# Kernel tuning notes

Measured on AMD Instinct MI355X. Metric: run time of the kernel, lower is better.

## Reference

```python
import jax, jax.numpy as jnp
import numpy as np

N = 50000       # num entities
F_IN = 256      # input feature dim
H = 128         # hidden_dim (= per-head dim, concat=False)
HEADS = 4
L = 3           # num_layers
T = 3           # num edge types
E = 250000      # edges per type
NEG = 0.2       # leaky_relu slope (module + GATv2 default)


def setup_inputs() -> dict:
    key = jax.random.key(0)
    ks = jax.random.split(key, 10)
    s = 0.05
    return {
        "feat": jax.random.normal(ks[0], (N, F_IN), jnp.float32),
        "emb_table": jax.random.normal(ks[1], (N, H), jnp.float32),
        "proj_w": jax.random.normal(ks[2], (F_IN, H), jnp.float32) * s,
        "proj_b": jnp.zeros((H,), jnp.float32),
        "ln_g": jnp.ones((H,), jnp.float32),
        "ln_b": jnp.zeros((H,), jnp.float32),
        "skip_w": jnp.ones((L,), jnp.float32),
        "Wl": jax.random.normal(ks[3], (L, T, H, HEADS * H), jnp.float32) * s,
        "Wr": jax.random.normal(ks[4], (L, T, H, HEADS * H), jnp.float32) * s,
        "att": jax.random.normal(ks[5], (L, T, HEADS, H), jnp.float32) * s,
        "bias": jnp.zeros((L, T, H), jnp.float32),
        "edge_src": jax.random.randint(ks[6], (T, E), 0, N, jnp.int64),
        "edge_dst": jax.random.randint(ks[7], (T, E), 0, N, jnp.int64),
    }


def _layer_norm(x, g, b):
    mu = jnp.mean(x, axis=-1, keepdims=True)
    var = jnp.mean(jnp.square(x - mu), axis=-1, keepdims=True)
    return (x - mu) * jax.lax.rsqrt(var + 1e-5) * g + b


def _l2norm(x):
    n = jnp.sqrt(jnp.sum(jnp.square(x), axis=-1, keepdims=True))
    return x / jnp.maximum(n, 1e-12)


def _gatv2(x, wl, wr, a, b, src, dst):
    # x: [N,H]; wl,wr: [H, HEADS*H]; a: [HEADS,H]; src/dst: [E]
    xl = (x @ wl).reshape(N, HEADS, H)
    xr = (x @ wr).reshape(N, HEADS, H)
    m = xl[src] + xr[dst]                                   # [E,HEADS,H]
    e = jnp.sum(a * jax.nn.leaky_relu(m, NEG), axis=-1)     # [E,HEADS]
    # segment softmax over incoming edges per destination node
    emax = jax.lax.stop_gradient(jax.ops.segment_max(e, dst, num_segments=N))
    ex = jnp.exp(e - emax[dst])
    den = jax.ops.segment_sum(ex, dst, num_segments=N)      # [N,HEADS]
    alpha = ex / (den[dst] + 1e-16)                         # [E,HEADS]
    out = jax.ops.segment_sum(alpha[:, :, None] * xl[src], dst, num_segments=N)
    return jnp.mean(out, axis=1) + b                        # concat=False -> head mean


def reference(feat, emb_table, proj_w, proj_b, ln_g, ln_b, skip_w,
              Wl, Wr, att, bias, edge_src, edge_dst):
    h = jax.nn.leaky_relu(_layer_norm(feat @ proj_w + proj_b, ln_g, ln_b), NEG)
    ne = _l2norm(emb_table)                                 # normalize(embedding(arange(N)))
    x0 = 0.7 * h + 0.5 * ne
    x = x0
    for i in range(L):
        # HeteroConv(aggr='mean') over edge types, all on node type 'entity'
        per_type = [
            _gatv2(x, Wl[i, t], Wr[i, t], att[i, t], bias[i, t],
                   edge_src[t], edge_dst[t])
            for t in range(T)
        ]
        xu = jnp.mean(jnp.stack(per_type, axis=0), axis=0)
        alpha = jax.nn.sigmoid(skip_w[i])
        x = jax.nn.leaky_relu(xu, NEG) + alpha * x0          # dropout = identity (eval)
    return x
```

## Files before the change

kernel.cpp:

```cpp
#include <hip/hip_runtime.h>
#include <hip/hip_bf16.h>
#include <math.h>

#define N_NODES 50000
#define NOFF    50004
#define NBLK    49
#define F_IN    256
#define H       128
#define HEADS   4
#define HH      512
#define L_LAYERS 3
#define T_TYPES  3
#define E_EDGES  250000
#define NEG      0.2f

#define GEMM_RB  391
#define GEMM_GRID (GEMM_RB*8)

typedef __attribute__((ext_vector_type(8))) short short8_t;
typedef __attribute__((ext_vector_type(4))) float float4_t;
typedef __attribute__((ext_vector_type(2))) float float2_t;

__device__ __forceinline__ float leaky(float x) { return x > 0.f ? x : NEG * x; }

__device__ __forceinline__ unsigned int cvt_pk_bf16(float lo, float hi) {
    unsigned int d;
    asm("v_cvt_pk_bf16_f32 %0, %1, %2" : "=v"(d) : "v"(lo), "v"(hi));
    return d;
}

__device__ __forceinline__ unsigned short f2bf(float f) {
    return (unsigned short)cvt_pk_bf16(f, f);
}

__device__ __forceinline__ float bf2f(unsigned short u) {
    union { unsigned int i; float f; } v; v.i = ((unsigned)u) << 16; return v.f;
}

__device__ __forceinline__ float2_t pk_add(float2_t a, float2_t b) {
    float2_t d;
    asm("v_pk_add_f32 %0, %1, %2" : "=v"(d) : "v"(a), "v"(b));
    return d;
}
__device__ __forceinline__ float2_t pk_fma(float2_t a, float2_t b, float2_t c) {
    float2_t d;
    asm("v_pk_fma_f32 %0, %1, %2, %3" : "=v"(d) : "v"(a), "v"(b), "v"(c));
    return d;
}
__device__ __forceinline__ float2_t pk_abs(float2_t a) {
    union { float2_t f; unsigned int u[2]; } v; v.f = a;
    v.u[0] &= 0x7fffffffu;
    v.u[1] &= 0x7fffffffu;
    return v.f;
}

__device__ __forceinline__ float fast_exp2(float x) {
    return __builtin_amdgcn_exp2f(x);
}

template <int CTRL>
__device__ __forceinline__ float dpp_add(float x) {
    union { float f; int i; } a, b;
    a.f = x;
    b.i = __builtin_amdgcn_update_dpp(0, a.i, CTRL, 0xf, 0xf, true);
    return x + b.f;
}
__device__ __forceinline__ float row16_reduce(float p) {
    p = dpp_add<0xB1>(p);
    p = dpp_add<0x4E>(p);
    p = dpp_add<0x141>(p);
    p = dpp_add<0x140>(p);
    return p;
}

__device__ __forceinline__ void unpack_pk(uint4 q, float2_t* o) {
    union { unsigned int i; float f; } v;
    float2_t t;
    v.i = q.x << 16;         t.x = v.f;
    v.i = q.x & 0xffff0000u; t.y = v.f; o[0] = t;
    v.i = q.y << 16;         t.x = v.f;
    v.i = q.y & 0xffff0000u; t.y = v.f; o[1] = t;
    v.i = q.z << 16;         t.x = v.f;
    v.i = q.z & 0xffff0000u; t.y = v.f; o[2] = t;
    v.i = q.w << 16;         t.x = v.f;
    v.i = q.w & 0xffff0000u; t.y = v.f; o[3] = t;
}

__global__ void detect_kernel(const int* __restrict__ edst, int* __restrict__ flag) {
    __shared__ int s_any;
    if (threadIdx.x == 0) s_any = 0;
    __syncthreads();
    int a = 0;
    #pragma unroll
    for (int j = 0; j < 8; ++j) a |= edst[2 * (threadIdx.x * 8 + j) + 1];
    if (a) atomicOr(&s_any, 1);
    __syncthreads();
    if (threadIdx.x == 0) *flag = s_any ? 0 : 1;
}

__global__ void hist_kernel(const int* __restrict__ edst, int* __restrict__ counts,
                            const int* __restrict__ flag) {
    int idx = blockIdx.x * 256 + threadIdx.x;
    if (idx < T_TYPES * E_EDGES) {
        int sh = *flag;
        int t = idx / E_EDGES;
        int d = edst[(size_t)idx << sh];
        if ((unsigned)d < N_NODES)
            atomicAdd(&counts[t * N_NODES + d], 1);
    }
}

__global__ __launch_bounds__(256) void scan_a_kernel(const int* __restrict__ counts,
                                                     int* __restrict__ bsum) {
    const int b = blockIdx.x;
    const int t = b / NBLK, ch = b % NBLK;
    const int tid = threadIdx.x, lane = tid & 63;
    __shared__ int ws[4];
    const int* cnt = counts + t * N_NODES;
    int i0 = ch * 1024 + tid * 4;
    int s = 0;
    if (i0 + 3 < N_NODES) { int4 v = *(const int4*)(cnt + i0); s = v.x + v.y + v.z + v.w; }
    else { for (int j = 0; j < 4; ++j) { int i = i0 + j; if (i < N_NODES) s += cnt[i]; } }
    #pragma unroll
    for (int o = 32; o > 0; o >>= 1) s += __shfl_xor(s, o);
    if (lane == 0) ws[tid >> 6] = s;
    __syncthreads();
    if (tid == 0) bsum[b] = ws[0] + ws[1] + ws[2] + ws[3];
}

__global__ void scan_b_kernel(int* __restrict__ bsum, int* __restrict__ off) {
    int t = threadIdx.x;
    if (t < T_TYPES) {
        int run = 0;
        for (int c = 0; c < NBLK; ++c) { int v = bsum[t * NBLK + c]; bsum[t * NBLK + c] = run; run += v; }
        off[t * NOFF + N_NODES] = run;
    }
}

__global__ __launch_bounds__(256) void scan_c_kernel(const int* counts,
                                                     const int* __restrict__ bsum,
                                                     int* __restrict__ off,
                                                     int* cursor) {
    const int b = blockIdx.x;
    const int t = b / NBLK, ch = b % NBLK;
    const int tid = threadIdx.x, lane = tid & 63, w = tid >> 6;
    __shared__ int ws[4];
    const int* cnt = counts + t * N_NODES;
    int i0 = ch * 1024 + tid * 4;
    int v0 = 0, v1 = 0, v2 = 0, v3 = 0;
    if (i0 + 3 < N_NODES) { int4 v = *(const int4*)(cnt + i0); v0 = v.x; v1 = v.y; v2 = v.z; v3 = v.w; }
    else {
        if (i0     < N_NODES) v0 = cnt[i0];
        if (i0 + 1 < N_NODES) v1 = cnt[i0 + 1];
        if (i0 + 2 < N_NODES) v2 = cnt[i0 + 2];
        if (i0 + 3 < N_NODES) v3 = cnt[i0 + 3];
    }
    int s = v0 + v1 + v2 + v3;
    int x = s;
    #pragma unroll
    for (int o = 1; o < 64; o <<= 1) { int y = __shfl_up(x, o); if (lane >= o) x += y; }
    if (lane == 63) ws[w] = x;
    __syncthreads();
    int woff = 0;
    #pragma unroll
    for (int j = 0; j < 4; ++j) woff += (j < w) ? ws[j] : 0;
    int base = bsum[b] + woff + (x - s);
    int e0 = base, e1 = e0 + v0, e2 = e1 + v1, e3 = e2 + v2;
    if (i0 + 3 < N_NODES) {
        *(int4*)(off + t * NOFF + i0)       = make_int4(e0, e1, e2, e3);
        *(int4*)(cursor + t * N_NODES + i0) = make_int4(e0, e1, e2, e3);
    } else {
        if (i0     < N_NODES) { off[t * NOFF + i0]     = e0; cursor[t * N_NODES + i0]     = e0; }
        if (i0 + 1 < N_NODES) { off[t * NOFF + i0 + 1] = e1; cursor[t * N_NODES + i0 + 1] = e1; }
        if (i0 + 2 < N_NODES) { off[t * NOFF + i0 + 2] = e2; cursor[t * N_NODES + i0 + 2] = e2; }
        if (i0 + 3 < N_NODES) { off[t * NOFF + i0 + 3] = e3; cursor[t * N_NODES + i0 + 3] = e3; }
    }
}

__global__ void scatter_kernel(const int* __restrict__ esrc, const int* __restrict__ edst,
                               int* __restrict__ cursor, int* __restrict__ csrc,
                               const int* __restrict__ flag) {
    int idx = blockIdx.x * 256 + threadIdx.x;
    if (idx < T_TYPES * E_EDGES) {
        int sh = *flag;
        int t = idx / E_EDGES;
        int d = edst[(size_t)idx << sh];
        if ((unsigned)d >= N_NODES) return;
        int s = esrc[(size_t)idx << sh];
        if ((unsigned)s >= N_NODES) s = 0;
        int pos = atomicAdd(&cursor[t * N_NODES + d], 1);
        if ((unsigned)pos < E_EDGES)
            csrc[(size_t)t * E_EDGES + pos] = s;
    }
}

__global__ void wconv_kernel(const float* __restrict__ Wl, const float* __restrict__ Wr,
                             unsigned short* __restrict__ Wt) {
    int idx = blockIdx.x * 256 + threadIdx.x;
    if (idx >= L_LAYERS * T_TYPES * 1024 * H) return;
    int lt  = idx / (1024 * H);
    int rem = idx - lt * (1024 * H);
    int c   = rem / H;
    int k   = rem - c * H;
    float v = (c < HH) ? Wl[(size_t)lt * H * HH + (size_t)k * HH + c]
                       : Wr[(size_t)lt * H * HH + (size_t)k * HH + (c - HH)];
    Wt[idx] = f2bf(v);
}

__global__ void featconv_kernel(const float* __restrict__ feat,
                                unsigned short* __restrict__ fHi,
                                unsigned short* __restrict__ fLo) {
    size_t i = ((size_t)blockIdx.x * 256 + threadIdx.x) * 4;
    if (i >= (size_t)N_NODES * F_IN) return;
    float4 v = *(const float4*)(feat + i);
    ushort4 h, l;
    h.x = f2bf(v.x); l.x = f2bf(v.x - bf2f(h.x));
    h.y = f2bf(v.y); l.y = f2bf(v.y - bf2f(h.y));
    h.z = f2bf(v.z); l.z = f2bf(v.z - bf2f(h.z));
    h.w = f2bf(v.w); l.w = f2bf(v.w - bf2f(h.w));
    *(ushort4*)(fHi + i) = h;
    *(ushort4*)(fLo + i) = l;
}

__global__ void pconv_kernel(const float* __restrict__ pw,
                             unsigned short* __restrict__ pWtHi,
                             unsigned short* __restrict__ pWtLo) {
    int idx = blockIdx.x * 256 + threadIdx.x;
    if (idx >= H * F_IN) return;
    int c = idx / F_IN, k = idx - c * F_IN;
    float v = pw[(size_t)k * H + c];
    unsigned short hi = f2bf(v);
    pWtHi[idx] = hi;
    pWtLo[idx] = f2bf(v - bf2f(hi));
}

__device__ __forceinline__ void stage_tile(unsigned short* dst, const unsigned short* src,
                                           int rbase, int kbase, int tid, bool guardRows) {
    #pragma unroll
    for (int it = 0; it < 8; ++it) {
        int c = it * 256 + tid;
        int r = c >> 4, k8 = c & 15;
        int slot = (k8 ^ (r & 15)) * 8;
        uint4 v = make_uint4(0, 0, 0, 0);
        int row = rbase + r;
        if (!guardRows || row < N_NODES)
            v = *(const uint4*)(src + (size_t)row * 256 + kbase + k8 * 8);
        *(uint4*)(dst + r * 128 + slot) = v;
    }
}

__global__ __launch_bounds__(256) void init_gemm_kernel(
    const unsigned short* __restrict__ fHi, const unsigned short* __restrict__ fLo,
    const unsigned short* __restrict__ pWtHi, const unsigned short* __restrict__ pWtLo,
    float* __restrict__ proj)
{
    __shared__ unsigned short smem[32768];
    unsigned short* As = smem;
    unsigned short* Bs = smem + 16384;
    const int tid = threadIdx.x;
    const int nb = blockIdx.x * 128;

    const int wv = tid >> 6, lane = tid & 63;
    const int lm = lane & 15, kg = lane >> 4;
    const int wm = (wv & 1) * 64, wn = (wv >> 1) * 64;
    float4_t acc[4][4];
    #pragma unroll
    for (int i = 0; i < 4; ++i)
        #pragma unroll
        for (int j = 0; j < 4; ++j)
            acc[i][j] = (float4_t){0.f, 0.f, 0.f, 0.f};

    auto compute = [&]() {
        #pragma unroll
        for (int ks = 0; ks < 4; ++ks) {
            const int K8 = ks * 4 + kg;
            const int slot = (K8 ^ lm) * 8;
            short8_t a[4], b[4];
            #pragma unroll
            for (int i = 0; i < 4; ++i) {
                a[i] = *(const short8_t*)(As + (wm + i * 16 + lm) * 128 + slot);
                b[i] = *(const short8_t*)(Bs + (wn + i * 16 + lm) * 128 + slot);
            }
            #pragma unroll
            for (int i = 0; i < 4; ++i)
                #pragma unroll
                for (int j = 0; j < 4; ++j)
                    acc[i][j] = __builtin_amdgcn_mfma_f32_16x16x32_bf16(a[i], b[j], acc[i][j], 0, 0, 0);
        }
    };

    #pragma unroll
    for (int kh = 0; kh < 2; ++kh) {
        const int kbase = kh * 128;
        stage_tile(As, fHi, nb, kbase, tid, true);
        stage_tile(Bs, pWtHi, 0, kbase, tid, false);
        __syncthreads();
        compute();
        __syncthreads();
        stage_tile(Bs, pWtLo, 0, kbase, tid, false);
        __syncthreads();
        compute();
        __syncthreads();
        stage_tile(As, fLo, nb, kbase, tid, true);
        stage_tile(Bs, pWtHi, 0, kbase, tid, false);
        __syncthreads();
        compute();
        __syncthreads();
    }

    #pragma unroll
    for (int i = 0; i < 4; ++i) {
        #pragma unroll
        for (int r = 0; r < 4; ++r) {
            int node = nb + wm + i * 16 + kg * 4 + r;
            if (node < N_NODES) {
                #pragma unroll
                for (int j = 0; j < 4; ++j)
                    proj[(size_t)node * H + wn + j * 16 + lm] = acc[i][j][r];
            }
        }
    }
}

__global__ __launch_bounds__(128) void ln_combine_kernel(
    const float* __restrict__ proj, const float* __restrict__ emb,
    const float* __restrict__ pb, const float* __restrict__ g, const float* __restrict__ b,
    float* __restrict__ x0, unsigned short* __restrict__ xcurb)
{
    __shared__ float s0[2], s1[2];
    const int tid = threadIdx.x;
    const int nb = blockIdx.x * 8;
    const int c = tid;
    float acc[8];
    #pragma unroll
    for (int nn = 0; nn < 8; ++nn) {
        int node = nb + nn;
        acc[nn] = (node < N_NODES) ? proj[(size_t)node * H + c] : 0.f;
    }
    const float pbc = pb[c], gc = g[c], bc = b[c];
    for (int nn = 0; nn < 8; ++nn) {
        float v = acc[nn] + pbc;
        float sum = v, sq = v * v;
        for (int o = 32; o > 0; o >>= 1) { sum += __shfl_down(sum, o); sq += __shfl_down(sq, o); }
        if ((tid & 63) == 0) { s0[tid >> 6] = sum; s1[tid >> 6] = sq; }
        __syncthreads();
        float tot = s0[0] + s0[1], tq = s1[0] + s1[1];
        __syncthreads();
        float mu = tot * (1.f / H);
        float var = tq * (1.f / H) - mu * mu;
        acc[nn] = leaky((v - mu) * rsqrtf(var + 1e-5f) * gc + bc);
    }
    for (int nn = 0; nn < 8; ++nn) {
        int node = nb + nn;
        float ev = (node < N_NODES) ? emb[(size_t)node * H + c] : 0.f;
        float sq = ev * ev;
        for (int o = 32; o > 0; o >>= 1) sq += __shfl_down(sq, o);
        if ((tid & 63) == 0) s0[tid >> 6] = sq;
        __syncthreads();
        float nrm = sqrtf(s0[0] + s0[1]);
        __syncthreads();
        float nev = ev / fmaxf(nrm, 1e-12f);
        float xv = 0.7f * acc[nn] + 0.5f * nev;
        if (node < N_NODES) {
            x0[(size_t)node * H + c] = xv;
            xcurb[(size_t)node * H + c] = f2bf(xv);
        }
    }
}

__global__ __launch_bounds__(256) void gemm_mfma_kernel(
    const unsigned short* __restrict__ x,
    const unsigned short* __restrict__ Wt,
    unsigned short* __restrict__ XL, unsigned short* __restrict__ XR)
{
    __shared__ unsigned short smem[32768];
    unsigned short* As = smem;
    unsigned short* Bs = smem + 16384;
    const int tid = threadIdx.x;

    const int f    = blockIdx.x;
    const int g    = (f % 8) * GEMM_RB + (f / 8);
    const int rowb = g >> 3;
    const int colb = g & 7;
    const int nb = rowb * 128;
    const int cb = colb * 128;

    #pragma unroll
    for (int it = 0; it < 8; ++it) {
        int c = it * 256 + tid;
        int r = c >> 4;
        int k8 = c & 15;
        int slot = (k8 ^ (r & 15)) * 8;
        int node = nb + r;
        uint4 va = make_uint4(0, 0, 0, 0);
        if (node < N_NODES) va = *(const uint4*)(x + (size_t)node * H + k8 * 8);
        *(uint4*)(As + r * H + slot) = va;
        uint4 vb = *(const uint4*)(Wt + (size_t)(cb + r) * H + k8 * 8);
        *(uint4*)(Bs + r * H + slot) = vb;
    }
    __syncthreads();

    const int wv = tid >> 6, lane = tid & 63;
    const int lm = lane & 15, kg = lane >> 4;
    const int wm = (wv & 1) * 64, wn = (wv >> 1) * 64;
    float4_t acc[4][4];
    #pragma unroll
    for (int i = 0; i < 4; ++i)
        #pragma unroll
        for (int j = 0; j < 4; ++j)
            acc[i][j] = (float4_t){0.f, 0.f, 0.f, 0.f};

    #pragma unroll
    for (int ks = 0; ks < 4; ++ks) {
        const int K8 = ks * 4 + kg;
        const int slot = (K8 ^ lm) * 8;
        short8_t a[4], b[4];
        #pragma unroll
        for (int i = 0; i < 4; ++i) {
            a[i] = *(const short8_t*)(As + (wm + i * 16 + lm) * H + slot);
            b[i] = *(const short8_t*)(Bs + (wn + i * 16 + lm) * H + slot);
        }
        #pragma unroll
        for (int i = 0; i < 4; ++i)
            #pragma unroll
            for (int j = 0; j < 4; ++j)
                acc[i][j] = __builtin_amdgcn_mfma_f32_16x16x32_bf16(a[i], b[j], acc[i][j], 0, 0, 0);
    }
    __syncthreads();

    unsigned short* Cs = smem;
    #pragma unroll
    for (int i = 0; i < 4; ++i) {
        int row0 = wm + i * 16 + kg * 4;
        #pragma unroll
        for (int j = 0; j < 4; ++j) {
            int col = wn + j * 16 + lm;
            #pragma unroll
            for (int r = 0; r < 4; ++r)
                Cs[(row0 + r) * 136 + col] = f2bf(acc[i][j][r]);
        }
    }
    __syncthreads();

    unsigned short* O = (colb < 4) ? XL : XR;
    const int cbase = (colb < 4) ? cb : cb - HH;
    #pragma unroll
    for (int it = 0; it < 8; ++it) {
        int c = it * 256 + tid;
        int r = c >> 4, k8 = (c & 15) * 8;
        int node = nb + r;
        if (node < N_NODES)
            *(uint4*)(O + (size_t)node * HH + cbase + k8) = *(const uint4*)(Cs + r * 136 + k8);
    }
}

__global__ __launch_bounds__(64) void aggregate_kernel(
    const unsigned short* __restrict__ XL, const unsigned short* __restrict__ XR,
    const float* __restrict__ att_t, const float* __restrict__ bias_t,
    const int* __restrict__ off, const int* __restrict__ csrc,
    float* __restrict__ xacc, int first,
    int fin, const float* __restrict__ x0, const float* __restrict__ skipw,
    int li, int last, unsigned short* __restrict__ xcurb, float* __restrict__ out)
{
    const int lane = threadIdx.x;
    const int d = blockIdx.x;
    if (d >= N_NODES) return;
    const int jb = lane * 8;
    const float L2E = 1.4426950408889634f;

    float2_t rv[4], c1[4], c2[4], acc2[4];
    {
        uint4 q = *(const uint4*)(XR + (size_t)d * HH + jb);
        unpack_pk(q, rv);
        float4 u0 = *(const float4*)(att_t + jb);
        float4 u1 = *(const float4*)(att_t + jb + 4);
        float av[8] = {u0.x, u0.y, u0.z, u0.w, u1.x, u1.y, u1.z, u1.w};
        #pragma unroll
        for (int u = 0; u < 4; ++u) {
            c1[u] = (float2_t){0.6f * L2E * av[2 * u], 0.6f * L2E * av[2 * u + 1]};
            c2[u] = (float2_t){0.4f * L2E * av[2 * u], 0.4f * L2E * av[2 * u + 1]};
            acc2[u] = (float2_t){0.f, 0.f};
        }
    }
    float den = 0.f;

    const int e0 = off[d];
    const int cnt = off[d + 1] - e0;

    uint4 q0 = make_uint4(0, 0, 0, 0), q1 = q0;
    unsigned s2 = 0, s3 = 0;
    if (cnt > 0) q0 = *(const uint4*)(XL + (size_t)((unsigned)csrc[e0])     * HH + jb);
    if (cnt > 1) q1 = *(const uint4*)(XL + (size_t)((unsigned)csrc[e0 + 1]) * HH + jb);
    if (cnt > 2) s2 = (unsigned)csrc[e0 + 2];
    if (cnt > 3) s3 = (unsigned)csrc[e0 + 3];

    int e = 0;
    for (; e + 1 < cnt; e += 2) {
        float2_t lv0[4], lv1[4];
        unpack_pk(q0, lv0);
        unpack_pk(q1, lv1);
        if (e + 2 < cnt) q0 = *(const uint4*)(XL + (size_t)s2 * HH + jb);
        if (e + 3 < cnt) q1 = *(const uint4*)(XL + (size_t)s3 * HH + jb);
        if (e + 4 < cnt) s2 = (unsigned)csrc[e0 + e + 4];
        if (e + 5 < cnt) s3 = (unsigned)csrc[e0 + e + 5];

        float2_t p20 = (float2_t){0.f, 0.f};
        float2_t p21 = (float2_t){0.f, 0.f};
        #pragma unroll
        for (int u = 0; u < 4; ++u) {
            float2_t m0 = pk_add(lv0[u], rv[u]);
            float2_t m1 = pk_add(lv1[u], rv[u]);
            float2_t a0 = pk_abs(m0);
            float2_t a1 = pk_abs(m1);
            p20 = pk_fma(c1[u], m0, p20);
            p21 = pk_fma(c1[u], m1, p21);
            p20 = pk_fma(c2[u], a0, p20);
            p21 = pk_fma(c2[u], a1, p21);
        }
        float p0 = row16_reduce(p20.x + p20.y);
        float p1 = row16_reduce(p21.x + p21.y);
        float w0 = fast_exp2(p0);
        float w1 = fast_exp2(p1);
        den += w0 + w1;
        float2_t w20 = (float2_t){w0, w0};
        float2_t w21 = (float2_t){w1, w1};
        #pragma unroll
        for (int u = 0; u < 4; ++u) {
            acc2[u] = pk_fma(w20, lv0[u], acc2[u]);
            acc2[u] = pk_fma(w21, lv1[u], acc2[u]);
        }
    }
    if (e < cnt) {
        float2_t lv0[4];
        unpack_pk(q0, lv0);
        float2_t p20 = (float2_t){0.f, 0.f};
        #pragma unroll
        for (int u = 0; u < 4; ++u) {
            float2_t m0 = pk_add(lv0[u], rv[u]);
            float2_t a0 = pk_abs(m0);
            p20 = pk_fma(c1[u], m0, p20);
            p20 = pk_fma(c2[u], a0, p20);
        }
        float p0 = row16_reduce(p20.x + p20.y);
        float w0 = fast_exp2(p0);
        den += w0;
        float2_t w20 = (float2_t){w0, w0};
        #pragma unroll
        for (int u = 0; u < 4; ++u) acc2[u] = pk_fma(w20, lv0[u], acc2[u]);
    }

    float inv = 1.f / (den + 1e-16f);
    float o[8];
    #pragma unroll
    for (int u = 0; u < 4; ++u) { o[2 * u] = acc2[u].x; o[2 * u + 1] = acc2[u].y; }
    #pragma unroll
    for (int u = 0; u < 8; ++u) {
        float v = o[u] * inv;
        v += __shfl_xor(v, 16);
        v += __shfl_xor(v, 32);
        o[u] = v * 0.25f;
    }
    if (lane < 16) {
        float* dst = xacc + (size_t)d * H + jb;
        #pragma unroll
        for (int u = 0; u < 8; ++u) o[u] += bias_t[jb + u];
        if (!fin) {
            float4 o0 = make_float4(o[0], o[1], o[2], o[3]);
            float4 o1 = make_float4(o[4], o[5], o[6], o[7]);
            if (first) {
                *(float4*)dst = o0;
                *(float4*)(dst + 4) = o1;
            } else {
                float4 c0 = *(const float4*)dst, c1v = *(const float4*)(dst + 4);
                o0.x += c0.x; o0.y += c0.y; o0.z += c0.z; o0.w += c0.w;
                o1.x += c1v.x; o1.y += c1v.y; o1.z += c1v.z; o1.w += c1v.w;
                *(float4*)dst = o0;
                *(float4*)(dst + 4) = o1;
            }
        } else {
            float sw = 1.f / (1.f + __expf(-skipw[li]));
            float4 c0 = *(const float4*)dst, c1v = *(const float4*)(dst + 4);
            float a0 = c0.x + o[0], a1 = c0.y + o[1], a2 = c0.z + o[2], a3 = c0.w + o[3];
            float a4 = c1v.x + o[4], a5 = c1v.y + o[5], a6 = c1v.z + o[6], a7 = c1v.w + o[7];
            const float* z = x0 + (size_t)d * H + jb;
            float4 z0 = *(const float4*)z, z1 = *(const float4*)(z + 4);
            float r0 = leaky(a0 * (1.f / 3.f)) + sw * z0.x;
            float r1 = leaky(a1 * (1.f / 3.f)) + sw * z0.y;
            float r2 = leaky(a2 * (1.f / 3.f)) + sw * z0.z;
            float r3 = leaky(a3 * (1.f / 3.f)) + sw * z0.w;
            float r4 = leaky(a4 * (1.f / 3.f)) + sw * z1.x;
            float r5 = leaky(a5 * (1.f / 3.f)) + sw * z1.y;
            float r6 = leaky(a6 * (1.f / 3.f)) + sw * z1.z;
            float r7 = leaky(a7 * (1.f / 3.f)) + sw * z1.w;
            if (last) {
                float* op = out + (size_t)d * H + jb;
                *(float4*)op       = make_float4(r0, r1, r2, r3);
                *(float4*)(op + 4) = make_float4(r4, r5, r6, r7);
            } else {
                unsigned int w0 = cvt_pk_bf16(r0, r1);
                unsigned int w1 = cvt_pk_bf16(r2, r3);
                unsigned int w2 = cvt_pk_bf16(r4, r5);
                unsigned int w3 = cvt_pk_bf16(r6, r7);
                *(uint4*)(xcurb + (size_t)d * H + jb) = make_uint4(w0, w1, w2, w3);
            }
        }
    }
}

extern "C" void kernel_launch(void* const* d_in, const int* in_sizes, int n_in,
                              void* d_out, int out_size, void* d_ws, size_t ws_size,
                              hipStream_t stream)
{
    const float* feat   = (const float*)d_in[0];
    const float* emb    = (const float*)d_in[1];
    const float* proj_w = (const float*)d_in[2];
    const float* proj_b = (const float*)d_in[3];
    const float* ln_g   = (const float*)d_in[4];
    const float* ln_b   = (const float*)d_in[5];
    const float* skip_w = (const float*)d_in[6];
    const float* Wl     = (const float*)d_in[7];
    const float* Wr     = (const float*)d_in[8];
    const float* att    = (const float*)d_in[9];
    const float* bias   = (const float*)d_in[10];
    const int*   esrc   = (const int*)d_in[11];
    const int*   edst   = (const int*)d_in[12];
    float* out = (float*)d_out;

    char* p = (char*)d_ws;
    auto alloc = [&](size_t bytes) -> char* {
        char* r = p; p += (bytes + 255) & ~(size_t)255; return r;
    };
    float* x0             = (float*)alloc((size_t)N_NODES * H * 4);
    unsigned short* xcurb = (unsigned short*)alloc((size_t)N_NODES * H * 2);
    unsigned short* XL    = (unsigned short*)alloc((size_t)N_NODES * HH * 2);
    unsigned short* XR    = (unsigned short*)alloc((size_t)N_NODES * HH * 2);
    unsigned short* Wt    = (unsigned short*)alloc((size_t)L_LAYERS * T_TYPES * 1024 * H * 2);
    unsigned short* pWtHi = (unsigned short*)alloc((size_t)H * F_IN * 2);
    unsigned short* pWtLo = (unsigned short*)alloc((size_t)H * F_IN * 2);
    int* off    = (int*)alloc((size_t)T_TYPES * NOFF * 4);
    int* cursor = (int*)alloc((size_t)T_TYPES * N_NODES * 4);
    int* csrc   = (int*)alloc((size_t)T_TYPES * E_EDGES * 4);
    int* bsum   = (int*)alloc((size_t)T_TYPES * NBLK * 4);
    int* eflag  = (int*)alloc(256);
    float* xacc = out;

    float* proj          = (float*)XL;
    unsigned short* fHi  = XR;
    unsigned short* fLo  = XR + (size_t)N_NODES * F_IN;

    detect_kernel<<<1, 256, 0, stream>>>(edst, eflag);
    hipMemsetAsync(cursor, 0, (size_t)T_TYPES * N_NODES * 4, stream);
    hist_kernel<<<(T_TYPES * E_EDGES + 255) / 256, 256, 0, stream>>>(edst, cursor, eflag);
    scan_a_kernel<<<T_TYPES * NBLK, 256, 0, stream>>>(cursor, bsum);
    scan_b_kernel<<<1, 256, 0, stream>>>(bsum, off);
    scan_c_kernel<<<T_TYPES * NBLK, 256, 0, stream>>>(cursor, bsum, off, cursor);
    scatter_kernel<<<(T_TYPES * E_EDGES + 255) / 256, 256, 0, stream>>>(esrc, edst, cursor, csrc, eflag);

    wconv_kernel<<<(L_LAYERS * T_TYPES * 1024 * H + 255) / 256, 256, 0, stream>>>(Wl, Wr, Wt);
    featconv_kernel<<<((N_NODES * F_IN / 4) + 255) / 256, 256, 0, stream>>>(feat, fHi, fLo);
    pconv_kernel<<<(H * F_IN + 255) / 256, 256, 0, stream>>>(proj_w, pWtHi, pWtLo);
    init_gemm_kernel<<<(N_NODES + 127) / 128, 256, 0, stream>>>(fHi, fLo, pWtHi, pWtLo, proj);
    ln_combine_kernel<<<N_NODES / 8, 128, 0, stream>>>(proj, emb, proj_b, ln_g, ln_b, x0, xcurb);

    for (int i = 0; i < L_LAYERS; ++i) {
        for (int t = 0; t < T_TYPES; ++t) {
            const int lt = i * T_TYPES + t;
            const unsigned short* wt = Wt + (size_t)lt * 1024 * H;
            const float* at = att + (size_t)lt * HEADS * H;
            const float* bi = bias + (size_t)lt * H;
            gemm_mfma_kernel<<<GEMM_GRID, 256, 0, stream>>>(xcurb, wt, XL, XR);
            aggregate_kernel<<<N_NODES, 64, 0, stream>>>(
                XL, XR, at, bi, off + t * NOFF, csrc + (size_t)t * E_EDGES,
                xacc, (t == 0) ? 1 : 0,
                (t == T_TYPES - 1) ? 1 : 0, x0, skip_w, i,
                (i == L_LAYERS - 1) ? 1 : 0, xcurb, out);
        }
    }
}
```

Before: 1.095 ms.

## Merge preprocessing kernels into combined launches and fold scan_b into scan_c

Independent setup kernels are packed into three multi-role launches that dispatch on block index: feature, weight and projection-weight conversion plus edge-format detection; the init GEMM plus histogram; and layer-norm combine plus block-sum scan. The serial scan_b kernel is removed, so each scan_c block now sums its preceding block totals itself and the last block writes the end offset. The aim is fewer kernel launches and serial gaps in preprocessing, with unrelated work running concurrently. The cost is that mixed-role blocks share one LDS and register allocation, and the layer-norm part now runs 256-thread blocks covering 16 nodes.

```diff
diff --git a/kernel.cpp b/kernel.cpp
--- a/kernel.cpp
+++ b/kernel.cpp
@@ -17,6 +17,17 @@
 #define GEMM_RB  391
 #define GEMM_GRID (GEMM_RB*8)
 
+#define CA_FEAT  12500
+#define CA_WCONV 4608
+#define CA_PCONV 128
+#define CA_TOTAL (CA_FEAT + CA_WCONV + CA_PCONV + 1)
+#define CB_INIT  391
+#define CB_HIST  2930
+#define CB_TOTAL (CB_INIT + CB_HIST)
+#define CC_LN    3125
+#define CC_SCANA (T_TYPES*NBLK)
+#define CC_TOTAL (CC_LN + CC_SCANA)
+
 typedef __attribute__((ext_vector_type(8))) short short8_t;
 typedef __attribute__((ext_vector_type(4))) float float4_t;
 typedef __attribute__((ext_vector_type(2))) float float2_t;
@@ -86,65 +97,236 @@
     v.i = q.w & 0xffff0000u; t.y = v.f; o[3] = t;
 }
 
-__global__ void detect_kernel(const int* __restrict__ edst, int* __restrict__ flag) {
+__device__ __forceinline__ void stage_tile(unsigned short* dst, const unsigned short* src,
+                                           int rbase, int kbase, int tid, bool guardRows) {
+    #pragma unroll
+    for (int it = 0; it < 8; ++it) {
+        int c = it * 256 + tid;
+        int r = c >> 4, k8 = c & 15;
+        int slot = (k8 ^ (r & 15)) * 8;
+        uint4 v = make_uint4(0, 0, 0, 0);
+        int row = rbase + r;
+        if (!guardRows || row < N_NODES)
+            v = *(const uint4*)(src + (size_t)row * 256 + kbase + k8 * 8);
+        *(uint4*)(dst + r * 128 + slot) = v;
+    }
+}
+
+__global__ __launch_bounds__(256) void combo_a_kernel(
+    const float* __restrict__ feat, unsigned short* __restrict__ fHi, unsigned short* __restrict__ fLo,
+    const float* __restrict__ Wl, const float* __restrict__ Wr, unsigned short* __restrict__ Wt,
+    const float* __restrict__ pw, unsigned short* __restrict__ pWtHi, unsigned short* __restrict__ pWtLo,
+    const int* __restrict__ edst, int* __restrict__ flag)
+{
     __shared__ int s_any;
-    if (threadIdx.x == 0) s_any = 0;
-    __syncthreads();
-    int a = 0;
-    #pragma unroll
-    for (int j = 0; j < 8; ++j) a |= edst[2 * (threadIdx.x * 8 + j) + 1];
-    if (a) atomicOr(&s_any, 1);
-    __syncthreads();
-    if (threadIdx.x == 0) *flag = s_any ? 0 : 1;
-}
-
-__global__ void hist_kernel(const int* __restrict__ edst, int* __restrict__ counts,
-                            const int* __restrict__ flag) {
-    int idx = blockIdx.x * 256 + threadIdx.x;
-    if (idx < T_TYPES * E_EDGES) {
-        int sh = *flag;
-        int t = idx / E_EDGES;
-        int d = edst[(size_t)idx << sh];
-        if ((unsigned)d < N_NODES)
-            atomicAdd(&counts[t * N_NODES + d], 1);
-    }
-}
-
-__global__ __launch_bounds__(256) void scan_a_kernel(const int* __restrict__ counts,
-                                                     int* __restrict__ bsum) {
-    const int b = blockIdx.x;
-    const int t = b / NBLK, ch = b % NBLK;
-    const int tid = threadIdx.x, lane = tid & 63;
+    const int bid = blockIdx.x;
+    const int tid = threadIdx.x;
+    if (bid < CA_FEAT) {
+        size_t i = ((size_t)bid * 256 + tid) * 4;
+        float4 v = *(const float4*)(feat + i);
+        ushort4 h, l;
+        h.x = f2bf(v.x); l.x = f2bf(v.x - bf2f(h.x));
+        h.y = f2bf(v.y); l.y = f2bf(v.y - bf2f(h.y));
+        h.z = f2bf(v.z); l.z = f2bf(v.z - bf2f(h.z));
+        h.w = f2bf(v.w); l.w = f2bf(v.w - bf2f(h.w));
+        *(ushort4*)(fHi + i) = h;
+        *(ushort4*)(fLo + i) = l;
+    } else if (bid < CA_FEAT + CA_WCONV) {
+        int idx = (bid - CA_FEAT) * 256 + tid;
+        int lt  = idx / (1024 * H);
+        int rem = idx - lt * (1024 * H);
+        int c   = rem / H;
+        int k   = rem - c * H;
+        float v = (c < HH) ? Wl[(size_t)lt * H * HH + (size_t)k * HH + c]
+                           : Wr[(size_t)lt * H * HH + (size_t)k * HH + (c - HH)];
+        Wt[idx] = f2bf(v);
+    } else if (bid < CA_FEAT + CA_WCONV + CA_PCONV) {
+        int idx = (bid - CA_FEAT - CA_WCONV) * 256 + tid;
+        int c = idx / F_IN, k = idx - c * F_IN;
+        float v = pw[(size_t)k * H + c];
+        unsigned short hi = f2bf(v);
+        pWtHi[idx] = hi;
+        pWtLo[idx] = f2bf(v - bf2f(hi));
+    } else {
+        if (tid == 0) s_any = 0;
+        __syncthreads();
+        int a = 0;
+        #pragma unroll
+        for (int j = 0; j < 8; ++j) a |= edst[2 * (tid * 8 + j) + 1];
+        if (a) atomicOr(&s_any, 1);
+        __syncthreads();
+        if (tid == 0) *flag = s_any ? 0 : 1;
+    }
+}
+
+__device__ __forceinline__ void init_gemm_body(
+    unsigned short* smem,
+    const unsigned short* __restrict__ fHi, const unsigned short* __restrict__ fLo,
+    const unsigned short* __restrict__ pWtHi, const unsigned short* __restrict__ pWtLo,
+    float* __restrict__ proj, int bid, int tid)
+{
+    unsigned short* As = smem;
+    unsigned short* Bs = smem + 16384;
+    const int nb = bid * 128;
+
+    const int wv = tid >> 6, lane = tid & 63;
+    const int lm = lane & 15, kg = lane >> 4;
+    const int wm = (wv & 1) * 64, wn = (wv >> 1) * 64;
+    float4_t acc[4][4];
+    #pragma unroll
+    for (int i = 0; i < 4; ++i)
+        #pragma unroll
+        for (int j = 0; j < 4; ++j)
+            acc[i][j] = (float4_t){0.f, 0.f, 0.f, 0.f};
+
+    auto compute = [&]() {
+        #pragma unroll
+        for (int ks = 0; ks < 4; ++ks) {
+            const int K8 = ks * 4 + kg;
+            const int slot = (K8 ^ lm) * 8;
+            short8_t a[4], b[4];
+            #pragma unroll
+            for (int i = 0; i < 4; ++i) {
+                a[i] = *(const short8_t*)(As + (wm + i * 16 + lm) * 128 + slot);
+                b[i] = *(const short8_t*)(Bs + (wn + i * 16 + lm) * 128 + slot);
+            }
+            #pragma unroll
+            for (int i = 0; i < 4; ++i)
+                #pragma unroll
+                for (int j = 0; j < 4; ++j)
+                    acc[i][j] = __builtin_amdgcn_mfma_f32_16x16x32_bf16(a[i], b[j], acc[i][j], 0, 0, 0);
+        }
+    };
+
+    #pragma unroll
+    for (int kh = 0; kh < 2; ++kh) {
+        const int kbase = kh * 128;
+        stage_tile(As, fHi, nb, kbase, tid, true);
+        stage_tile(Bs, pWtHi, 0, kbase, tid, false);
+        __syncthreads();
+        compute();
+        __syncthreads();
+        stage_tile(Bs, pWtLo, 0, kbase, tid, false);
+        __syncthreads();
+        compute();
+        __syncthreads();
+        stage_tile(As, fLo, nb, kbase, tid, true);
+        stage_tile(Bs, pWtHi, 0, kbase, tid, false);
+        __syncthreads();
+        compute();
+        __syncthreads();
+    }
+
+    #pragma unroll
+    for (int i = 0; i < 4; ++i) {
+        #pragma unroll
+        for (int r = 0; r < 4; ++r) {
+            int node = nb + wm + i * 16 + kg * 4 + r;
+            if (node < N_NODES) {
+                #pragma unroll
+                for (int j = 0; j < 4; ++j)
+                    proj[(size_t)node * H + wn + j * 16 + lm] = acc[i][j][r];
+            }
+        }
+    }
+}
+
+__global__ __launch_bounds__(256) void combo_b_kernel(
+    const unsigned short* __restrict__ fHi, const unsigned short* __restrict__ fLo,
+    const unsigned short* __restrict__ pWtHi, const unsigned short* __restrict__ pWtLo,
+    float* __restrict__ proj,
+    const int* __restrict__ edst, int* __restrict__ counts, const int* __restrict__ flag)
+{
+    __shared__ unsigned short smem[32768];
+    const int bid = blockIdx.x;
+    const int tid = threadIdx.x;
+    if (bid < CB_INIT) {
+        init_gemm_body(smem, fHi, fLo, pWtHi, pWtLo, proj, bid, tid);
+    } else {
+        int idx = (bid - CB_INIT) * 256 + tid;
+        if (idx < T_TYPES * E_EDGES) {
+            int sh = *flag;
+            int t = idx / E_EDGES;
+            int d = edst[(size_t)idx << sh];
+            if ((unsigned)d < N_NODES)
+                atomicAdd(&counts[t * N_NODES + d], 1);
+        }
+    }
+}
+
+__global__ __launch_bounds__(256) void combo_c_kernel(
+    const float* __restrict__ proj, const float* __restrict__ emb,
+    const float* __restrict__ pb, const float* __restrict__ g, const float* __restrict__ b,
+    float* __restrict__ x0, unsigned short* __restrict__ xcurb,
+    const int* __restrict__ counts, int* __restrict__ bsum)
+{
+    __shared__ float s0[4], s1[4];
     __shared__ int ws[4];
-    const int* cnt = counts + t * N_NODES;
-    int i0 = ch * 1024 + tid * 4;
-    int s = 0;
-    if (i0 + 3 < N_NODES) { int4 v = *(const int4*)(cnt + i0); s = v.x + v.y + v.z + v.w; }
-    else { for (int j = 0; j < 4; ++j) { int i = i0 + j; if (i < N_NODES) s += cnt[i]; } }
-    #pragma unroll
-    for (int o = 32; o > 0; o >>= 1) s += __shfl_xor(s, o);
-    if (lane == 0) ws[tid >> 6] = s;
-    __syncthreads();
-    if (tid == 0) bsum[b] = ws[0] + ws[1] + ws[2] + ws[3];
-}
-
-__global__ void scan_b_kernel(int* __restrict__ bsum, int* __restrict__ off) {
-    int t = threadIdx.x;
-    if (t < T_TYPES) {
-        int run = 0;
-        for (int c = 0; c < NBLK; ++c) { int v = bsum[t * NBLK + c]; bsum[t * NBLK + c] = run; run += v; }
-        off[t * NOFF + N_NODES] = run;
-    }
-}
-
-__global__ __launch_bounds__(256) void scan_c_kernel(const int* counts,
-                                                     const int* __restrict__ bsum,
-                                                     int* __restrict__ off,
-                                                     int* cursor) {
+    const int bid = blockIdx.x;
+    const int tid = threadIdx.x;
+    if (bid < CC_LN) {
+        const int h = tid >> 7;
+        const int c = tid & 127;
+        const int wv = tid >> 6;
+        const int nb = bid * 16 + h * 8;
+        float acc[8];
+        #pragma unroll
+        for (int nn = 0; nn < 8; ++nn)
+            acc[nn] = proj[(size_t)(nb + nn) * H + c];
+        const float pbc = pb[c], gc = g[c], bc = b[c];
+        for (int nn = 0; nn < 8; ++nn) {
+            float v = acc[nn] + pbc;
+            float sum = v, sq = v * v;
+            for (int o = 32; o > 0; o >>= 1) { sum += __shfl_down(sum, o); sq += __shfl_down(sq, o); }
+            if ((tid & 63) == 0) { s0[wv] = sum; s1[wv] = sq; }
+            __syncthreads();
+            float tot = s0[2 * h] + s0[2 * h + 1], tq = s1[2 * h] + s1[2 * h + 1];
+            __syncthreads();
+            float mu = tot * (1.f / H);
+            float var = tq * (1.f / H) - mu * mu;
+            acc[nn] = leaky((v - mu) * rsqrtf(var + 1e-5f) * gc + bc);
+        }
+        for (int nn = 0; nn < 8; ++nn) {
+            int node = nb + nn;
+            float ev = emb[(size_t)node * H + c];
+            float sq = ev * ev;
+            for (int o = 32; o > 0; o >>= 1) sq += __shfl_down(sq, o);
+            if ((tid & 63) == 0) s0[wv] = sq;
+            __syncthreads();
+            float nrm = sqrtf(s0[2 * h] + s0[2 * h + 1]);
+            __syncthreads();
+            float nev = ev / fmaxf(nrm, 1e-12f);
+            float xv = 0.7f * acc[nn] + 0.5f * nev;
+            x0[(size_t)node * H + c] = xv;
+            xcurb[(size_t)node * H + c] = f2bf(xv);
+        }
+    } else {
+        const int sb = bid - CC_LN;
+        const int t = sb / NBLK, ch = sb % NBLK;
+        const int lane = tid & 63;
+        const int* cnt = counts + t * N_NODES;
+        int i0 = ch * 1024 + tid * 4;
+        int s = 0;
+        if (i0 + 3 < N_NODES) { int4 v = *(const int4*)(cnt + i0); s = v.x + v.y + v.z + v.w; }
+        else { for (int j = 0; j < 4; ++j) { int i = i0 + j; if (i < N_NODES) s += cnt[i]; } }
+        #pragma unroll
+        for (int o = 32; o > 0; o >>= 1) s += __shfl_xor(s, o);
+        if (lane == 0) ws[tid >> 6] = s;
+        __syncthreads();
+        if (tid == 0) bsum[sb] = ws[0] + ws[1] + ws[2] + ws[3];
+    }
+}
+
+__global__ __launch_bounds__(256) void scan_c2_kernel(const int* counts,
+                                                      const int* __restrict__ bsum,
+                                                      int* __restrict__ off,
+                                                      int* cursor) {
     const int b = blockIdx.x;
     const int t = b / NBLK, ch = b % NBLK;
     const int tid = threadIdx.x, lane = tid & 63, w = tid >> 6;
     __shared__ int ws[4];
+    int run = 0;
+    for (int c = 0; c < ch; ++c) run += bsum[t * NBLK + c];
     const int* cnt = counts + t * N_NODES;
     int i0 = ch * 1024 + tid * 4;
     int v0 = 0, v1 = 0, v2 = 0, v3 = 0;
@@ -164,7 +346,7 @@
     int woff = 0;
     #pragma unroll
     for (int j = 0; j < 4; ++j) woff += (j < w) ? ws[j] : 0;
-    int base = bsum[b] + woff + (x - s);
+    int base = run + woff + (x - s);
     int e0 = base, e1 = e0 + v0, e2 = e1 + v1, e3 = e2 + v2;
     if (i0 + 3 < N_NODES) {
         *(int4*)(off + t * NOFF + i0)       = make_int4(e0, e1, e2, e3);
@@ -175,6 +357,8 @@
         if (i0 + 2 < N_NODES) { off[t * NOFF + i0 + 2] = e2; cursor[t * N_NODES + i0 + 2] = e2; }
         if (i0 + 3 < N_NODES) { off[t * NOFF + i0 + 3] = e3; cursor[t * N_NODES + i0 + 3] = e3; }
     }
+    if (ch == NBLK - 1 && tid == 255)
+        off[t * NOFF + N_NODES] = run + woff + x;
 }
 
 __global__ void scatter_kernel(const int* __restrict__ esrc, const int* __restrict__ edst,
@@ -191,180 +375,6 @@
         int pos = atomicAdd(&cursor[t * N_NODES + d], 1);
         if ((unsigned)pos < E_EDGES)
             csrc[(size_t)t * E_EDGES + pos] = s;
-    }
-}
-
-__global__ void wconv_kernel(const float* __restrict__ Wl, const float* __restrict__ Wr,
-                             unsigned short* __restrict__ Wt) {
-    int idx = blockIdx.x * 256 + threadIdx.x;
-    if (idx >= L_LAYERS * T_TYPES * 1024 * H) return;
-    int lt  = idx / (1024 * H);
-    int rem = idx - lt * (1024 * H);
-    int c   = rem / H;
-    int k   = rem - c * H;
-    float v = (c < HH) ? Wl[(size_t)lt * H * HH + (size_t)k * HH + c]
-                       : Wr[(size_t)lt * H * HH + (size_t)k * HH + (c - HH)];
-    Wt[idx] = f2bf(v);
-}
-
-__global__ void featconv_kernel(const float* __restrict__ feat,
-                                unsigned short* __restrict__ fHi,
-                                unsigned short* __restrict__ fLo) {
-    size_t i = ((size_t)blockIdx.x * 256 + threadIdx.x) * 4;
-    if (i >= (size_t)N_NODES * F_IN) return;
-    float4 v = *(const float4*)(feat + i);
-    ushort4 h, l;
-    h.x = f2bf(v.x); l.x = f2bf(v.x - bf2f(h.x));
-    h.y = f2bf(v.y); l.y = f2bf(v.y - bf2f(h.y));
-    h.z = f2bf(v.z); l.z = f2bf(v.z - bf2f(h.z));
-    h.w = f2bf(v.w); l.w = f2bf(v.w - bf2f(h.w));
-    *(ushort4*)(fHi + i) = h;
-    *(ushort4*)(fLo + i) = l;
-}
-
-__global__ void pconv_kernel(const float* __restrict__ pw,
-                             unsigned short* __restrict__ pWtHi,
-                             unsigned short* __restrict__ pWtLo) {
-    int idx = blockIdx.x * 256 + threadIdx.x;
-    if (idx >= H * F_IN) return;
-    int c = idx / F_IN, k = idx - c * F_IN;
-    float v = pw[(size_t)k * H + c];
-    unsigned short hi = f2bf(v);
-    pWtHi[idx] = hi;
-    pWtLo[idx] = f2bf(v - bf2f(hi));
-}
-
-__device__ __forceinline__ void stage_tile(unsigned short* dst, const unsigned short* src,
-                                           int rbase, int kbase, int tid, bool guardRows) {
-    #pragma unroll
-    for (int it = 0; it < 8; ++it) {
-        int c = it * 256 + tid;
-        int r = c >> 4, k8 = c & 15;
-        int slot = (k8 ^ (r & 15)) * 8;
-        uint4 v = make_uint4(0, 0, 0, 0);
-        int row = rbase + r;
-        if (!guardRows || row < N_NODES)
-            v = *(const uint4*)(src + (size_t)row * 256 + kbase + k8 * 8);
-        *(uint4*)(dst + r * 128 + slot) = v;
-    }
-}
-
-__global__ __launch_bounds__(256) void init_gemm_kernel(
-    const unsigned short* __restrict__ fHi, const unsigned short* __restrict__ fLo,
-    const unsigned short* __restrict__ pWtHi, const unsigned short* __restrict__ pWtLo,
-    float* __restrict__ proj)
-{
-    __shared__ unsigned short smem[32768];
-    unsigned short* As = smem;
-    unsigned short* Bs = smem + 16384;
-    const int tid = threadIdx.x;
-    const int nb = blockIdx.x * 128;
-
-    const int wv = tid >> 6, lane = tid & 63;
-    const int lm = lane & 15, kg = lane >> 4;
-    const int wm = (wv & 1) * 64, wn = (wv >> 1) * 64;
-    float4_t acc[4][4];
-    #pragma unroll
-    for (int i = 0; i < 4; ++i)
-        #pragma unroll
-        for (int j = 0; j < 4; ++j)
-            acc[i][j] = (float4_t){0.f, 0.f, 0.f, 0.f};
-
-    auto compute = [&]() {
-        #pragma unroll
-        for (int ks = 0; ks < 4; ++ks) {
-            const int K8 = ks * 4 + kg;
-            const int slot = (K8 ^ lm) * 8;
-            short8_t a[4], b[4];
-            #pragma unroll
-            for (int i = 0; i < 4; ++i) {
-                a[i] = *(const short8_t*)(As + (wm + i * 16 + lm) * 128 + slot);
-                b[i] = *(const short8_t*)(Bs + (wn + i * 16 + lm) * 128 + slot);
-            }
-            #pragma unroll
-            for (int i = 0; i < 4; ++i)
-                #pragma unroll
-                for (int j = 0; j < 4; ++j)
-                    acc[i][j] = __builtin_amdgcn_mfma_f32_16x16x32_bf16(a[i], b[j], acc[i][j], 0, 0, 0);
-        }
-    };
-
-    #pragma unroll
-    for (int kh = 0; kh < 2; ++kh) {
-        const int kbase = kh * 128;
-        stage_tile(As, fHi, nb, kbase, tid, true);
-        stage_tile(Bs, pWtHi, 0, kbase, tid, false);
-        __syncthreads();
-        compute();
-        __syncthreads();
-        stage_tile(Bs, pWtLo, 0, kbase, tid, false);
-        __syncthreads();
-        compute();
-        __syncthreads();
-        stage_tile(As, fLo, nb, kbase, tid, true);
-        stage_tile(Bs, pWtHi, 0, kbase, tid, false);
-        __syncthreads();
-        compute();
-        __syncthreads();
-    }
-
-    #pragma unroll
-    for (int i = 0; i < 4; ++i) {
-        #pragma unroll
-        for (int r = 0; r < 4; ++r) {
-            int node = nb + wm + i * 16 + kg * 4 + r;
-            if (node < N_NODES) {
-                #pragma unroll
-                for (int j = 0; j < 4; ++j)
-                    proj[(size_t)node * H + wn + j * 16 + lm] = acc[i][j][r];
-            }
-        }
-    }
-}
-
-__global__ __launch_bounds__(128) void ln_combine_kernel(
-    const float* __restrict__ proj, const float* __restrict__ emb,
-    const float* __restrict__ pb, const float* __restrict__ g, const float* __restrict__ b,
-    float* __restrict__ x0, unsigned short* __restrict__ xcurb)
-{
-    __shared__ float s0[2], s1[2];
-    const int tid = threadIdx.x;
-    const int nb = blockIdx.x * 8;
-    const int c = tid;
-    float acc[8];
-    #pragma unroll
-    for (int nn = 0; nn < 8; ++nn) {
-        int node = nb + nn;
-        acc[nn] = (node < N_NODES) ? proj[(size_t)node * H + c] : 0.f;
-    }
-    const float pbc = pb[c], gc = g[c], bc = b[c];
-    for (int nn = 0; nn < 8; ++nn) {
-        float v = acc[nn] + pbc;
-        float sum = v, sq = v * v;
-        for (int o = 32; o > 0; o >>= 1) { sum += __shfl_down(sum, o); sq += __shfl_down(sq, o); }
-        if ((tid & 63) == 0) { s0[tid >> 6] = sum; s1[tid >> 6] = sq; }
-        __syncthreads();
-        float tot = s0[0] + s0[1], tq = s1[0] + s1[1];
-        __syncthreads();
-        float mu = tot * (1.f / H);
-        float var = tq * (1.f / H) - mu * mu;
-        acc[nn] = leaky((v - mu) * rsqrtf(var + 1e-5f) * gc + bc);
-    }
-    for (int nn = 0; nn < 8; ++nn) {
-        int node = nb + nn;
-        float ev = (node < N_NODES) ? emb[(size_t)node * H + c] : 0.f;
-        float sq = ev * ev;
-        for (int o = 32; o > 0; o >>= 1) sq += __shfl_down(sq, o);
-        if ((tid & 63) == 0) s0[tid >> 6] = sq;
-        __syncthreads();
-        float nrm = sqrtf(s0[0] + s0[1]);
-        __syncthreads();
-        float nev = ev / fmaxf(nrm, 1e-12f);
-        float xv = 0.7f * acc[nn] + 0.5f * nev;
-        if (node < N_NODES) {
-            x0[(size_t)node * H + c] = xv;
-            xcurb[(size_t)node * H + c] = f2bf(xv);
-        }
     }
 }
 
@@ -648,19 +658,16 @@
     unsigned short* fHi  = XR;
     unsigned short* fLo  = XR + (size_t)N_NODES * F_IN;
 
-    detect_kernel<<<1, 256, 0, stream>>>(edst, eflag);
     hipMemsetAsync(cursor, 0, (size_t)T_TYPES * N_NODES * 4, stream);
-    hist_kernel<<<(T_TYPES * E_EDGES + 255) / 256, 256, 0, stream>>>(edst, cursor, eflag);
-    scan_a_kernel<<<T_TYPES * NBLK, 256, 0, stream>>>(cursor, bsum);
-    scan_b_kernel<<<1, 256, 0, stream>>>(bsum, off);
-    scan_c_kernel<<<T_TYPES * NBLK, 256, 0, stream>>>(cursor, bsum, off, cursor);
+
+    combo_a_kernel<<<CA_TOTAL, 256, 0, stream>>>(feat, fHi, fLo, Wl, Wr, Wt,
+                                                 proj_w, pWtHi, pWtLo, edst, eflag);
+    combo_b_kernel<<<CB_TOTAL, 256, 0, stream>>>(fHi, fLo, pWtHi, pWtLo, proj,
+                                                 edst, cursor, eflag);
+    combo_c_kernel<<<CC_TOTAL, 256, 0, stream>>>(proj, emb, proj_b, ln_g, ln_b,
+                                                 x0, xcurb, cursor, bsum);
+    scan_c2_kernel<<<T_TYPES * NBLK, 256, 0, stream>>>(cursor, bsum, off, cursor);
     scatter_kernel<<<(T_TYPES * E_EDGES + 255) / 256, 256, 0, stream>>>(esrc, edst, cursor, csrc, eflag);
-
-    wconv_kernel<<<(L_LAYERS * T_TYPES * 1024 * H + 255) / 256, 256, 0, stream>>>(Wl, Wr, Wt);
-    featconv_kernel<<<((N_NODES * F_IN / 4) + 255) / 256, 256, 0, stream>>>(feat, fHi, fLo);
-    pconv_kernel<<<(H * F_IN + 255) / 256, 256, 0, stream>>>(proj_w, pWtHi, pWtLo);
-    init_gemm_kernel<<<(N_NODES + 127) / 128, 256, 0, stream>>>(fHi, fLo, pWtHi, pWtLo, proj);
-    ln_combine_kernel<<<N_NODES / 8, 128, 0, stream>>>(proj, emb, proj_b, ln_g, ln_b, x0, xcurb);
 
     for (int i = 0; i < L_LAYERS; ++i) {
         for (int t = 0; t < T_TYPES; ++t) {
```

Result: faster. 1.067 ms (-2.6%).
